# Kernel tuning notes

Hardware: AMD Instinct MI355X
Metric: run time of the kernel (lower is better)

## Reference

```python
import jax, jax.numpy as jnp
import numpy as np

B, LQ, LK = 1, 2048, 2048
D, H, KVH, DH = 4096, 32, 8, 128
G = H // KVH  # head groups


def setup_inputs() -> dict:
    key = jax.random.key(0)
    ks = jax.random.split(key, 7)
    s = 0.02
    hidden_q = jax.random.normal(ks[0], (B, LQ, D), dtype=jnp.float32)
    hidden_kv = jax.random.normal(ks[1], (B, LK, D), dtype=jnp.float32)
    # causal boolean mask (batch, len_q, len_k)
    attention_mask = jnp.broadcast_to(jnp.tril(jnp.ones((LQ, LK), dtype=bool)), (B, LQ, LK))
    position_bias = jax.random.normal(ks[2], (H, LQ, LK), dtype=jnp.float32) * 0.1
    Wq = jax.random.normal(ks[3], (D, H * DH), dtype=jnp.float32) * s
    Wk = jax.random.normal(ks[4], (D, KVH * DH), dtype=jnp.float32) * s
    Wv = jax.random.normal(ks[5], (D, KVH * DH), dtype=jnp.float32) * s
    Wo = jax.random.normal(ks[6], (H * DH, D), dtype=jnp.float32) * s
    return {"hidden_q": hidden_q, "hidden_kv": hidden_kv,
            "attention_mask": attention_mask, "position_bias": position_bias,
            "Wq": Wq, "Wk": Wk, "Wv": Wv, "Wo": Wo}


def reference(hidden_q, hidden_kv, attention_mask, position_bias, Wq, Wk, Wv, Wo):
    inv4 = DH ** -0.25  # q and k each scaled by dim_head**-1/4
    q = (hidden_q @ Wq) * inv4            # [B, LQ, H*DH]
    k = (hidden_kv @ Wk) * inv4           # [B, LK, KVH*DH]
    v = hidden_kv @ Wv                     # [B, LK, KVH*DH]
    q = q.reshape(B, LQ, KVH, G, DH)       # group heads for GQA
    k = k.reshape(B, LK, KVH, DH)
    v = v.reshape(B, LK, KVH, DH)
    # score: [B, KVH, G, LQ, LK] -> [B, H, LQ, LK]
    score = jnp.einsum('bqkgd,blkd->bkgql', q, k).reshape(B, H, LQ, LK)
    score = score + position_bias[None]
    mask = attention_mask[:, None]         # [B, 1, LQ, LK]
    score = jnp.where(mask, score, -jnp.inf)
    p = jax.nn.softmax(score, axis=-1)
    p = jnp.where(mask, p, 0.0)
    out = jnp.einsum('bkgql,blkd->bqkgd', p.reshape(B, KVH, G, LQ, LK), v)
    out = out.reshape(B, LQ, H * DH) @ Wo  # [B, LQ, D]
    return out
```

## Files before the change

kernel.cpp:

```cpp
#include <hip/hip_runtime.h>
#include <hip/hip_bf16.h>
#include <cstdint>
#include <cstddef>

typedef __attribute__((ext_vector_type(4))) float f32x4;
typedef __attribute__((ext_vector_type(4))) short s16x4;
typedef __attribute__((ext_vector_type(8))) short s16x8;

#define SLQ 2048
#define SLK 2048
#define SNH 32
#define SDH 128

__device__ __forceinline__ short f2bf(float x) {
  unsigned u = __builtin_bit_cast(unsigned, x);
  u += 0x7FFF + ((u >> 16) & 1);
  return (short)(u >> 16);
}

__device__ __forceinline__ void gload_lds16(const void* g, const void* l) {
  __builtin_amdgcn_global_load_lds((const __attribute__((address_space(1))) void*)g,
                                   (__attribute__((address_space(3))) void*)l,
                                   16, 0, 0);
}

template<int CTRL>
__device__ __forceinline__ float dpp_f32(float x) {
  return __builtin_bit_cast(float, __builtin_amdgcn_update_dpp(
      0, __builtin_bit_cast(int, x), CTRL, 0xF, 0xF, true));
}
__device__ __forceinline__ float rowmax16(float x) {
  x = fmaxf(x, dpp_f32<0x128>(x));
  x = fmaxf(x, dpp_f32<0x124>(x));
  x = fmaxf(x, dpp_f32<0x122>(x));
  x = fmaxf(x, dpp_f32<0x121>(x));
  return x;
}
__device__ __forceinline__ float rowsum16(float x) {
  x += dpp_f32<0x128>(x);
  x += dpp_f32<0x124>(x);
  x += dpp_f32<0x122>(x);
  x += dpp_f32<0x121>(x);
  return x;
}

__global__ void convert_bf16_2(const float* __restrict__ in0, short* __restrict__ out0,
                               const float* __restrict__ in1, short* __restrict__ out1) {
  const int i = blockIdx.x * 256 + threadIdx.x;
  const float* in = blockIdx.y ? in1 : in0;
  short* out = blockIdx.y ? out1 : out0;
  f32x4 a = ((const f32x4*)in)[i];
  s16x4 b;
  b[0] = f2bf(a[0]); b[1] = f2bf(a[1]); b[2] = f2bf(a[2]); b[3] = f2bf(a[3]);
  ((s16x4*)out)[i] = b;
}

__global__ void transpose_all(const float* __restrict__ Wq, const float* __restrict__ Wo,
                              const float* __restrict__ Wk, const float* __restrict__ Wv,
                              short* __restrict__ WqT, short* __restrict__ WoT,
                              short* __restrict__ WkT, short* __restrict__ WvT) {
  __shared__ short T[64][68];
  const int K = 4096;
  int bx = blockIdx.x;
  const float* W; short* Wt; int N;
  if (bx < 64)       { W = Wq; Wt = WqT; N = 4096; }
  else if (bx < 128) { W = Wo; Wt = WoT; N = 4096; bx -= 64; }
  else if (bx < 144) { W = Wk; Wt = WkT; N = 1024; bx -= 128; }
  else               { W = Wv; Wt = WvT; N = 1024; bx -= 144; }
  const int tid = threadIdx.x;
  const int k0 = blockIdx.y * 64, n0 = bx * 64;
  const int r = tid >> 4;
  const int c4 = (tid & 15) * 4;
#pragma unroll
  for (int i = 0; i < 4; ++i) {
    f32x4 a = *(const f32x4*)(W + (size_t)(k0 + r + i * 16) * N + n0 + c4);
#pragma unroll
    for (int j = 0; j < 4; ++j) T[c4 + j][r + i * 16] = f2bf(a[j]);
  }
  __syncthreads();
  const int rn = tid >> 3;
  const int c8 = (tid & 7) * 8;
#pragma unroll
  for (int i = 0; i < 2; ++i) {
    s16x4 v0 = *(const s16x4*)&T[rn + i * 32][c8];
    s16x4 v1 = *(const s16x4*)&T[rn + i * 32][c8 + 4];
    short* dst = Wt + (size_t)(n0 + rn + i * 32) * K + k0 + c8;
    *(s16x4*)dst = v0;
    *(s16x4*)(dst + 4) = v1;
  }
}

template<int CM>
__global__ __launch_bounds__(512, 1)
void gemm_big(const short* __restrict__ A, const short* __restrict__ Bt,
              void* __restrict__ Cv, float scale) {
  __shared__ short As[3][128 * 64];
  __shared__ short Bs[3][256 * 64];
  const int N = 4096, K = 4096;
  const int tid = threadIdx.x, lane = tid & 63, w = tid >> 6;
  const int l15 = lane & 15, lg = lane >> 4;
  const int wr = w >> 2, wc = w & 3;
  const int nbx = N >> 8;
  const int nwg = gridDim.x, b = blockIdx.x;
  const int wg = (b & 7) * (nwg >> 3) + (b >> 3);
  const int m0 = (wg / nbx) * 128, n0 = (wg % nbx) * 256;

  f32x4 acc[4][4];
#pragma unroll
  for (int a = 0; a < 4; ++a)
#pragma unroll
    for (int c = 0; c < 4; ++c)
      acc[a][c] = (f32x4){0.f, 0.f, 0.f, 0.f};

#define GSTAGE(T, BUF) do {                                                    \
    _Pragma("unroll") for (int i_ = 0; i_ < 2; ++i_) {                         \
      const int ci = i_ * 512 + tid, r_ = ci >> 3, c_ = ci & 7;                \
      gload_lds16(A + (size_t)(m0 + r_) * K + (T) * 64 + ((c_ ^ (r_ & 7)) * 8),\
                  (const short*)As[BUF] + ci * 8); }                           \
    _Pragma("unroll") for (int i_ = 0; i_ < 4; ++i_) {                         \
      const int ci = i_ * 512 + tid, r_ = ci >> 3, c_ = ci & 7;                \
      gload_lds16(Bt + (size_t)(n0 + r_) * K + (T) * 64 + ((c_ ^ (r_ & 7)) * 8),\
                  (const short*)Bs[BUF] + ci * 8); }                           \
  } while (0)

  const int NT = K >> 6;
  GSTAGE(0, 0); GSTAGE(1, 1); GSTAGE(2, 2);
  int buf = 0;
  for (int t = 0; t < NT; ++t) {
    if (t + 2 < NT)      asm volatile("s_waitcnt vmcnt(12)" ::: "memory");
    else if (t + 1 < NT) asm volatile("s_waitcnt vmcnt(6)" ::: "memory");
    else                 asm volatile("s_waitcnt vmcnt(0)" ::: "memory");
    __builtin_amdgcn_s_barrier();
    const short* Ab = As[buf];
    const short* Bb = Bs[buf];
    s16x8 af[2][4], bfv[2][4];
#pragma unroll
    for (int kk = 0; kk < 2; ++kk) {
#pragma unroll
      for (int mi = 0; mi < 4; ++mi) {
        const int r = wr * 64 + mi * 16 + l15;
        const int c = (kk * 4 + lg) ^ (r & 7);
        af[kk][mi] = *(const s16x8*)(Ab + (r * 8 + c) * 8);
      }
#pragma unroll
      for (int ni = 0; ni < 4; ++ni) {
        const int r = wc * 64 + ni * 16 + l15;
        const int c = (kk * 4 + lg) ^ (r & 7);
        bfv[kk][ni] = *(const s16x8*)(Bb + (r * 8 + c) * 8);
      }
    }
    __builtin_amdgcn_s_setprio(1);
#pragma unroll
    for (int kk = 0; kk < 2; ++kk)
#pragma unroll
      for (int mi = 0; mi < 4; ++mi)
#pragma unroll
        for (int ni = 0; ni < 4; ++ni)
          acc[mi][ni] = __builtin_amdgcn_mfma_f32_16x16x32_bf16(af[kk][mi], bfv[kk][ni], acc[mi][ni], 0, 0, 0);
    __builtin_amdgcn_s_setprio(0);
    __builtin_amdgcn_s_barrier();
    if (t + 3 < NT) GSTAGE(t + 3, buf);
    buf = (buf == 2) ? 0 : buf + 1;
  }
#undef GSTAGE
#pragma unroll
  for (int mi = 0; mi < 4; ++mi) {
#pragma unroll
    for (int ni = 0; ni < 4; ++ni) {
#pragma unroll
      for (int j = 0; j < 4; ++j) {
        const int rg = m0 + wr * 64 + mi * 16 + lg * 4 + j;
        const int cg = n0 + wc * 64 + ni * 16 + l15;
        const float vv = acc[mi][ni][j] * scale;
        if (CM == 0) ((short*)Cv)[(size_t)rg * N + cg] = f2bf(vv);
        else         ((float*)Cv)[(size_t)rg * N + cg] = vv;
      }
    }
  }
}

__global__ __launch_bounds__(256, 2)
void gemm_kv(const short* __restrict__ A, const short* __restrict__ Bt,
             short* __restrict__ kout, short* __restrict__ vTout, float inv4) {
  __shared__ short As[128][32];
  __shared__ short Bs[128][32];
  const int N = 2048, K = 4096;
  const int tid = threadIdx.x, lane = tid & 63, wid = tid >> 6;
  const int l15 = lane & 15, lg = lane >> 4;
  const int nbx = N >> 7;
  const int nwg = gridDim.x, b = blockIdx.x;
  const int wg = (b & 7) * (nwg >> 3) + (b >> 3);
  const int m0 = (wg / nbx) * 128, n0 = (wg % nbx) * 128;
  const int wm = (wid >> 1) * 64, wn = (wid & 1) * 64;

  f32x4 acc[4][4];
#pragma unroll
  for (int a = 0; a < 4; ++a)
#pragma unroll
    for (int c = 0; c < 4; ++c)
      acc[a][c] = (f32x4){0.f, 0.f, 0.f, 0.f};

  for (int k0 = 0; k0 < K; k0 += 32) {
#pragma unroll
    for (int i = 0; i < 2; ++i) {
      const int c = i * 256 + wid * 64 + lane;
      const int rr = c >> 2, hh = (c & 3) * 8;
      gload_lds16(A  + (size_t)(m0 + rr) * K + k0 + hh,
                  (const short*)As + (size_t)(i * 256 + wid * 64) * 8);
      gload_lds16(Bt + (size_t)(n0 + rr) * K + k0 + hh,
                  (const short*)Bs + (size_t)(i * 256 + wid * 64) * 8);
    }
    __syncthreads();
    s16x8 af[4], bf[4];
#pragma unroll
    for (int mi = 0; mi < 4; ++mi)
      af[mi] = *(const s16x8*)&As[wm + mi * 16 + l15][lg * 8];
#pragma unroll
    for (int ni = 0; ni < 4; ++ni)
      bf[ni] = *(const s16x8*)&Bs[wn + ni * 16 + l15][lg * 8];
#pragma unroll
    for (int mi = 0; mi < 4; ++mi)
#pragma unroll
      for (int ni = 0; ni < 4; ++ni)
        acc[mi][ni] = __builtin_amdgcn_mfma_f32_16x16x32_bf16(af[mi], bf[ni], acc[mi][ni], 0, 0, 0);
    __syncthreads();
  }
  if (n0 < 1024) {
#pragma unroll
    for (int mi = 0; mi < 4; ++mi)
#pragma unroll
      for (int ni = 0; ni < 4; ++ni)
#pragma unroll
        for (int j = 0; j < 4; ++j) {
          const int rg = m0 + wm + mi * 16 + lg * 4 + j;
          const int cg = n0 + wn + ni * 16 + l15;
          kout[(size_t)rg * 1024 + cg] = f2bf(acc[mi][ni][j] * inv4);
        }
  } else {
#pragma unroll
    for (int mi = 0; mi < 4; ++mi)
#pragma unroll
      for (int ni = 0; ni < 4; ++ni) {
        s16x4 wv;
#pragma unroll
        for (int j = 0; j < 4; ++j) wv[j] = f2bf(acc[mi][ni][j]);
        const int rg0 = m0 + wm + mi * 16 + lg * 4;
        const int cg = n0 + wn + ni * 16 + l15 - 1024;
        *(s16x4*)(vTout + (size_t)cg * 2048 + rg0) = wv;
      }
  }
}

__global__ __launch_bounds__(256, 2)
void attn_kernel(const short* __restrict__ q, const short* __restrict__ k,
                 const short* __restrict__ vT, const float* __restrict__ bias,
                 short* __restrict__ o) {
  __shared__ __align__(16) short Ks[64 * 128];
  __shared__ __align__(16) short Vs[2][128 * 64];
  __shared__ __align__(16) short Ps[4][16][72];
  const int tid = threadIdx.x, lane = tid & 63, w = tid >> 6;
  const int l15 = lane & 15, lg = lane >> 4;
  const int b = blockIdx.x;
  const int h = b & 31;
  const int qt = 31 - (b >> 5);
  const int kvh = h >> 2;
  const int nt = qt + 1;

#define STAGE_K(IT) do { const int kv0_ = (IT) * 64;                          \
    _Pragma("unroll") for (int i_ = 0; i_ < 4; ++i_) {                        \
      const int ci = i_ * 256 + tid, r_ = ci >> 4, c_ = ci & 15;              \
      gload_lds16(k + (size_t)(kv0_ + r_) * 1024 + kvh * 128 + ((c_ ^ (r_ & 7)) * 8), \
                  (const short*)Ks + ci * 8); } } while (0)

#define STAGE_V(IT, P) do { const int kv0_ = (IT) * 64;                       \
    _Pragma("unroll") for (int i_ = 0; i_ < 4; ++i_) {                        \
      const int ci = i_ * 256 + tid, r_ = ci >> 3, c_ = ci & 7;               \
      gload_lds16(vT + (size_t)(kvh * 128 + r_) * 2048 + kv0_ + ((c_ ^ (r_ & 7)) * 8), \
                  (const short*)Vs[P] + ci * 8); } } while (0)

  const int qrow0 = qt * 64 + w * 16 + lg * 4;

#define LOAD_BIAS(IT, BB) do { const float* bp_ = bias + ((size_t)h * SLQ + qrow0) * SLK + (IT) * 64 + l15; \
    _Pragma("unroll") for (int ni_ = 0; ni_ < 4; ++ni_)                       \
      _Pragma("unroll") for (int j_ = 0; j_ < 4; ++j_)                        \
        BB[ni_][j_] = bp_[(size_t)j_ * SLK + ni_ * 16]; } while (0)

  s16x8 qf[4];
  {
    const short* qp = q + (size_t)(qt * 64 + w * 16 + l15) * (SNH * SDH) + h * SDH + lg * 8;
#pragma unroll
    for (int kk = 0; kk < 4; ++kk) qf[kk] = *(const s16x8*)(qp + kk * 32);
  }
  float mrow[4], lrow[4];
  f32x4 oacc[8];
#pragma unroll
  for (int j = 0; j < 4; ++j) { mrow[j] = -1e30f; lrow[j] = 0.f; }
#pragma unroll
  for (int nd = 0; nd < 8; ++nd) oacc[nd] = (f32x4){0.f, 0.f, 0.f, 0.f};

  float bbA[4][4], bbB[4][4];

  STAGE_V(0, 0);
  STAGE_K(0);
  LOAD_BIAS(0, bbA);
  if (nt > 1) LOAD_BIAS(1, bbB);

#define BODY(IT, BB) do {                                                     \
    const int p_ = (IT) & 1;                                                  \
    const int kv0_ = (IT) * 64;                                               \
    if ((IT) + 1 < nt) asm volatile("s_waitcnt vmcnt(16)" ::: "memory");      \
    else               asm volatile("s_waitcnt vmcnt(0)"  ::: "memory");      \
    __builtin_amdgcn_s_barrier();                                             \
    if ((IT) + 1 < nt) STAGE_V((IT) + 1, p_ ^ 1);                             \
    f32x4 s[4];                                                               \
    __builtin_amdgcn_s_setprio(1);                                            \
    _Pragma("unroll") for (int ni = 0; ni < 4; ++ni) {                        \
      s[ni] = (f32x4){0.f, 0.f, 0.f, 0.f};                                    \
      const int r = ni * 16 + l15;                                            \
      _Pragma("unroll") for (int kk = 0; kk < 4; ++kk) {                      \
        const int cc = kk * 4 + lg;                                           \
        s16x8 kf = *(const s16x8*)(Ks + (r * 16 + (cc ^ (r & 7))) * 8);       \
        s[ni] = __builtin_amdgcn_mfma_f32_16x16x32_bf16(qf[kk], kf, s[ni], 0, 0, 0); \
      }                                                                       \
    }                                                                         \
    __builtin_amdgcn_s_setprio(0);                                            \
    _Pragma("unroll") for (int ni = 0; ni < 4; ++ni) {                        \
      _Pragma("unroll") for (int j = 0; j < 4; ++j) {                         \
        float sv = s[ni][j] + BB[ni][j];                                      \
        if ((IT) == qt && kv0_ + ni * 16 + l15 > qrow0 + j) sv = -1e30f;      \
        s[ni][j] = sv;                                                        \
      }                                                                       \
    }                                                                         \
    float pmax[4];                                                            \
    _Pragma("unroll") for (int j = 0; j < 4; ++j) {                           \
      float mx = fmaxf(fmaxf(s[0][j], s[1][j]), fmaxf(s[2][j], s[3][j]));     \
      pmax[j] = rowmax16(mx);                                                 \
    }                                                                         \
    bool need = (pmax[0] > mrow[0] + 8.f) | (pmax[1] > mrow[1] + 8.f) |       \
                (pmax[2] > mrow[2] + 8.f) | (pmax[3] > mrow[3] + 8.f);        \
    if (__any(need)) {                                                        \
      _Pragma("unroll") for (int j = 0; j < 4; ++j) {                         \
        const float mn = fmaxf(mrow[j], pmax[j]);                             \
        const float fsj = __expf(mrow[j] - mn);                               \
        mrow[j] = mn;                                                         \
        lrow[j] *= fsj;                                                       \
        _Pragma("unroll") for (int nd = 0; nd < 8; ++nd) oacc[nd][j] *= fsj;  \
      }                                                                       \
    }                                                                         \
    float ps[4] = {0.f, 0.f, 0.f, 0.f};                                       \
    _Pragma("unroll") for (int ni = 0; ni < 4; ++ni)                          \
      _Pragma("unroll") for (int j = 0; j < 4; ++j) {                         \
        const float pv = __expf(s[ni][j] - mrow[j]);                          \
        s[ni][j] = pv;                                                        \
        ps[j] += pv;                                                          \
      }                                                                       \
    _Pragma("unroll") for (int j = 0; j < 4; ++j) lrow[j] += rowsum16(ps[j]); \
    __builtin_amdgcn_s_barrier();                                             \
    if ((IT) + 1 < nt) STAGE_K((IT) + 1);                                     \
    if ((IT) + 2 < nt) LOAD_BIAS((IT) + 2, BB);                               \
    _Pragma("unroll") for (int ni = 0; ni < 4; ++ni)                          \
      _Pragma("unroll") for (int j = 0; j < 4; ++j)                           \
        Ps[w][lg * 4 + j][ni * 16 + l15] = f2bf(s[ni][j]);                    \
    __builtin_amdgcn_s_setprio(1);                                            \
    _Pragma("unroll") for (int kk2 = 0; kk2 < 2; ++kk2) {                     \
      s16x8 pa = *(const s16x8*)&Ps[w][l15][kk2 * 32 + lg * 8];               \
      _Pragma("unroll") for (int nd = 0; nd < 8; ++nd) {                      \
        const int r = nd * 16 + l15;                                          \
        const int cc = kk2 * 4 + lg;                                          \
        s16x8 vf = *(const s16x8*)(Vs[p_] + (r * 8 + (cc ^ (r & 7))) * 8);    \
        oacc[nd] = __builtin_amdgcn_mfma_f32_16x16x32_bf16(pa, vf, oacc[nd], 0, 0, 0); \
      }                                                                       \
    }                                                                         \
    __builtin_amdgcn_s_setprio(0);                                            \
  } while (0)

  for (int it = 0; it < nt; ) {
    BODY(it, bbA);
    ++it;
    if (it < nt) { BODY(it, bbB); ++it; }
  }
#undef BODY
#undef STAGE_K
#undef STAGE_V
#undef LOAD_BIAS

#pragma unroll
  for (int j = 0; j < 4; ++j) {
    const float inv = 1.f / lrow[j];
    short* op = o + (size_t)(qrow0 + j) * (SNH * SDH) + h * SDH + l15;
#pragma unroll
    for (int nd = 0; nd < 8; ++nd)
      op[nd * 16] = f2bf(oacc[nd][j] * inv);
  }
}

extern "C" void kernel_launch(void* const* d_in, const int* in_sizes, int n_in,
                              void* d_out, int out_size, void* d_ws, size_t ws_size,
                              hipStream_t stream) {
  (void)in_sizes; (void)n_in; (void)out_size; (void)ws_size;
  const float* hq   = (const float*)d_in[0];
  const float* hkv  = (const float*)d_in[1];
  const float* bias = (const float*)d_in[3];
  const float* Wq   = (const float*)d_in[4];
  const float* Wk   = (const float*)d_in[5];
  const float* Wv   = (const float*)d_in[6];
  const float* Wo   = (const float*)d_in[7];

  short* ws = (short*)d_ws;
  const size_t MEG = 1048576;
  short* hqb  = ws;
  short* hkvb = ws + 8 * MEG;
  short* WT   = ws + 16 * MEG;
  short* WoT  = ws + 32 * MEG;
  short* WkvT = ws + 48 * MEG;
  short* qb   = ws + 56 * MEG;
  short* kb   = ws + 64 * MEG;
  short* vbT  = ws + 66 * MEG;
  short* ob   = hqb;

  const float inv4 = 0.29730177875068026f;

  convert_bf16_2<<<dim3(8192, 2), 256, 0, stream>>>(hq, hqb, hkv, hkvb);
  transpose_all<<<dim3(160, 64), 256, 0, stream>>>(
      Wq, Wo, Wk, Wv, WT, WoT, WkvT, WkvT + (size_t)1024 * 4096);

  gemm_big<0><<<256, 512, 0, stream>>>(hqb, WT, qb, inv4);
  gemm_kv<<<256, 256, 0, stream>>>(hkvb, WkvT, kb, vbT, inv4);

  attn_kernel<<<1024, 256, 0, stream>>>(qb, kb, vbT, bias, ob);

  gemm_big<1><<<256, 512, 0, stream>>>(ob, WoT, (float*)d_out, 1.0f);
}
```

Before: 472.7 us.

## Process two query heads per attention block sharing K/V tiles

The attention kernel now has each block handle two heads of the same KV group. K and V tiles loaded into LDS are reused across both heads, and the grid is halved to 512 blocks. The weight transpose and input conversion kernels are split into separate launches so the Wo workspace can be reused, and the GEMM tile-to-block mapping is changed to a fixed XCD-aware layout. This trades extra register pressure and fewer blocks for less K/V traffic, plus a few more kernel launches.

```diff
diff --git a/kernel.cpp b/kernel.cpp
--- a/kernel.cpp
+++ b/kernel.cpp
@@ -44,31 +44,21 @@
   return x;
 }
 
-__global__ void convert_bf16_2(const float* __restrict__ in0, short* __restrict__ out0,
-                               const float* __restrict__ in1, short* __restrict__ out1) {
-  const int i = blockIdx.x * 256 + threadIdx.x;
-  const float* in = blockIdx.y ? in1 : in0;
-  short* out = blockIdx.y ? out1 : out0;
-  f32x4 a = ((const f32x4*)in)[i];
-  s16x4 b;
-  b[0] = f2bf(a[0]); b[1] = f2bf(a[1]); b[2] = f2bf(a[2]); b[3] = f2bf(a[3]);
-  ((s16x4*)out)[i] = b;
-}
-
-__global__ void transpose_all(const float* __restrict__ Wq, const float* __restrict__ Wo,
-                              const float* __restrict__ Wk, const float* __restrict__ Wv,
-                              short* __restrict__ WqT, short* __restrict__ WoT,
-                              short* __restrict__ WkT, short* __restrict__ WvT) {
+__global__ void convert_bf16(const float* __restrict__ in, short* __restrict__ out, int n4) {
+  int i = blockIdx.x * 256 + threadIdx.x;
+  if (i < n4) {
+    f32x4 a = ((const f32x4*)in)[i];
+    s16x4 b;
+    b[0] = f2bf(a[0]); b[1] = f2bf(a[1]); b[2] = f2bf(a[2]); b[3] = f2bf(a[3]);
+    ((s16x4*)out)[i] = b;
+  }
+}
+
+__global__ void transpose_convert(const float* __restrict__ W, short* __restrict__ Wt,
+                                  int K, int N) {
   __shared__ short T[64][68];
-  const int K = 4096;
-  int bx = blockIdx.x;
-  const float* W; short* Wt; int N;
-  if (bx < 64)       { W = Wq; Wt = WqT; N = 4096; }
-  else if (bx < 128) { W = Wo; Wt = WoT; N = 4096; bx -= 64; }
-  else if (bx < 144) { W = Wk; Wt = WkT; N = 1024; bx -= 128; }
-  else               { W = Wv; Wt = WvT; N = 1024; bx -= 144; }
   const int tid = threadIdx.x;
-  const int k0 = blockIdx.y * 64, n0 = bx * 64;
+  const int k0 = blockIdx.y * 64, n0 = blockIdx.x * 64;
   const int r = tid >> 4;
   const int c4 = (tid & 15) * 4;
 #pragma unroll
@@ -100,10 +90,10 @@
   const int tid = threadIdx.x, lane = tid & 63, w = tid >> 6;
   const int l15 = lane & 15, lg = lane >> 4;
   const int wr = w >> 2, wc = w & 3;
-  const int nbx = N >> 8;
-  const int nwg = gridDim.x, b = blockIdx.x;
-  const int wg = (b & 7) * (nwg >> 3) + (b >> 3);
-  const int m0 = (wg / nbx) * 128, n0 = (wg % nbx) * 256;
+  const int b = blockIdx.x;
+  const int cp = b & 7, wi = b >> 3;
+  const int m0 = (wi >> 1) * 128;
+  const int n0 = (cp * 2 + (wi & 1)) * 256;
 
   f32x4 acc[4][4];
 #pragma unroll
@@ -261,9 +251,11 @@
   const int tid = threadIdx.x, lane = tid & 63, w = tid >> 6;
   const int l15 = lane & 15, lg = lane >> 4;
   const int b = blockIdx.x;
-  const int h = b & 31;
-  const int qt = 31 - (b >> 5);
-  const int kvh = h >> 2;
+  const int hp = b & 15;
+  const int qt = 31 - (b >> 4);
+  const int kvh = hp >> 1;
+  const int hA = kvh * 4 + (hp & 1) * 2;
+  const int hB = hA + 1;
   const int nt = qt + 1;
 
 #define STAGE_K(IT) do { const int kv0_ = (IT) * 64;                          \
@@ -280,39 +272,40 @@
 
   const int qrow0 = qt * 64 + w * 16 + lg * 4;
 
-#define LOAD_BIAS(IT, BB) do { const float* bp_ = bias + ((size_t)h * SLQ + qrow0) * SLK + (IT) * 64 + l15; \
+  float bbA[4][4], bbB[4][4];
+#define LOAD_BIAS(IT, BB, H) do { const float* bp_ = bias + ((size_t)(H) * SLQ + qrow0) * SLK + (IT) * 64 + l15; \
     _Pragma("unroll") for (int ni_ = 0; ni_ < 4; ++ni_)                       \
       _Pragma("unroll") for (int j_ = 0; j_ < 4; ++j_)                        \
         BB[ni_][j_] = bp_[(size_t)j_ * SLK + ni_ * 16]; } while (0)
 
-  s16x8 qf[4];
+  s16x8 qfA[4], qfB[4];
   {
-    const short* qp = q + (size_t)(qt * 64 + w * 16 + l15) * (SNH * SDH) + h * SDH + lg * 8;
-#pragma unroll
-    for (int kk = 0; kk < 4; ++kk) qf[kk] = *(const s16x8*)(qp + kk * 32);
-  }
-  float mrow[4], lrow[4];
-  f32x4 oacc[8];
-#pragma unroll
-  for (int j = 0; j < 4; ++j) { mrow[j] = -1e30f; lrow[j] = 0.f; }
-#pragma unroll
-  for (int nd = 0; nd < 8; ++nd) oacc[nd] = (f32x4){0.f, 0.f, 0.f, 0.f};
-
-  float bbA[4][4], bbB[4][4];
+    const short* qp = q + (size_t)(qt * 64 + w * 16 + l15) * (SNH * SDH) + lg * 8;
+#pragma unroll
+    for (int kk = 0; kk < 4; ++kk) {
+      qfA[kk] = *(const s16x8*)(qp + hA * SDH + kk * 32);
+      qfB[kk] = *(const s16x8*)(qp + hB * SDH + kk * 32);
+    }
+  }
+  float mrowA[4], lrowA[4], mrowB[4], lrowB[4];
+  f32x4 oaccA[8], oaccB[8];
+#pragma unroll
+  for (int j = 0; j < 4; ++j) {
+    mrowA[j] = -1e30f; lrowA[j] = 0.f;
+    mrowB[j] = -1e30f; lrowB[j] = 0.f;
+  }
+#pragma unroll
+  for (int nd = 0; nd < 8; ++nd) {
+    oaccA[nd] = (f32x4){0.f, 0.f, 0.f, 0.f};
+    oaccB[nd] = (f32x4){0.f, 0.f, 0.f, 0.f};
+  }
 
   STAGE_V(0, 0);
   STAGE_K(0);
-  LOAD_BIAS(0, bbA);
-  if (nt > 1) LOAD_BIAS(1, bbB);
-
-#define BODY(IT, BB) do {                                                     \
-    const int p_ = (IT) & 1;                                                  \
-    const int kv0_ = (IT) * 64;                                               \
-    if ((IT) + 1 < nt) asm volatile("s_waitcnt vmcnt(16)" ::: "memory");      \
-    else               asm volatile("s_waitcnt vmcnt(0)"  ::: "memory");      \
-    __builtin_amdgcn_s_barrier();                                             \
-    if ((IT) + 1 < nt) STAGE_V((IT) + 1, p_ ^ 1);                             \
-    f32x4 s[4];                                                               \
+  LOAD_BIAS(0, bbA, hA);
+  LOAD_BIAS(0, bbB, hB);
+
+#define QK_SM(QF, BB, MROW, LROW, OACC) do {                                  \
     __builtin_amdgcn_s_setprio(1);                                            \
     _Pragma("unroll") for (int ni = 0; ni < 4; ++ni) {                        \
       s[ni] = (f32x4){0.f, 0.f, 0.f, 0.f};                                    \
@@ -320,14 +313,14 @@
       _Pragma("unroll") for (int kk = 0; kk < 4; ++kk) {                      \
         const int cc = kk * 4 + lg;                                           \
         s16x8 kf = *(const s16x8*)(Ks + (r * 16 + (cc ^ (r & 7))) * 8);       \
-        s[ni] = __builtin_amdgcn_mfma_f32_16x16x32_bf16(qf[kk], kf, s[ni], 0, 0, 0); \
+        s[ni] = __builtin_amdgcn_mfma_f32_16x16x32_bf16(QF[kk], kf, s[ni], 0, 0, 0); \
       }                                                                       \
     }                                                                         \
     __builtin_amdgcn_s_setprio(0);                                            \
     _Pragma("unroll") for (int ni = 0; ni < 4; ++ni) {                        \
       _Pragma("unroll") for (int j = 0; j < 4; ++j) {                         \
         float sv = s[ni][j] + BB[ni][j];                                      \
-        if ((IT) == qt && kv0_ + ni * 16 + l15 > qrow0 + j) sv = -1e30f;      \
+        if (it == qt && kv0 + ni * 16 + l15 > qrow0 + j) sv = -1e30f;         \
         s[ni][j] = sv;                                                        \
       }                                                                       \
     }                                                                         \
@@ -336,61 +329,81 @@
       float mx = fmaxf(fmaxf(s[0][j], s[1][j]), fmaxf(s[2][j], s[3][j]));     \
       pmax[j] = rowmax16(mx);                                                 \
     }                                                                         \
-    bool need = (pmax[0] > mrow[0] + 8.f) | (pmax[1] > mrow[1] + 8.f) |       \
-                (pmax[2] > mrow[2] + 8.f) | (pmax[3] > mrow[3] + 8.f);        \
+    bool need = (pmax[0] > MROW[0] + 8.f) | (pmax[1] > MROW[1] + 8.f) |       \
+                (pmax[2] > MROW[2] + 8.f) | (pmax[3] > MROW[3] + 8.f);        \
     if (__any(need)) {                                                        \
       _Pragma("unroll") for (int j = 0; j < 4; ++j) {                         \
-        const float mn = fmaxf(mrow[j], pmax[j]);                             \
-        const float fsj = __expf(mrow[j] - mn);                               \
-        mrow[j] = mn;                                                         \
-        lrow[j] *= fsj;                                                       \
-        _Pragma("unroll") for (int nd = 0; nd < 8; ++nd) oacc[nd][j] *= fsj;  \
+        const float mn = fmaxf(MROW[j], pmax[j]);                             \
+        const float fsj = __expf(MROW[j] - mn);                               \
+        MROW[j] = mn;                                                         \
+        LROW[j] *= fsj;                                                       \
+        _Pragma("unroll") for (int nd = 0; nd < 8; ++nd) OACC[nd][j] *= fsj;  \
       }                                                                       \
     }                                                                         \
     float ps[4] = {0.f, 0.f, 0.f, 0.f};                                       \
     _Pragma("unroll") for (int ni = 0; ni < 4; ++ni)                          \
       _Pragma("unroll") for (int j = 0; j < 4; ++j) {                         \
-        const float pv = __expf(s[ni][j] - mrow[j]);                          \
+        const float pv = __expf(s[ni][j] - MROW[j]);                          \
         s[ni][j] = pv;                                                        \
         ps[j] += pv;                                                          \
       }                                                                       \
-    _Pragma("unroll") for (int j = 0; j < 4; ++j) lrow[j] += rowsum16(ps[j]); \
-    __builtin_amdgcn_s_barrier();                                             \
-    if ((IT) + 1 < nt) STAGE_K((IT) + 1);                                     \
-    if ((IT) + 2 < nt) LOAD_BIAS((IT) + 2, BB);                               \
+    _Pragma("unroll") for (int j = 0; j < 4; ++j) LROW[j] += rowsum16(ps[j]); \
+  } while (0)
+
+#define PV(S, OACC, P) do {                                                   \
     _Pragma("unroll") for (int ni = 0; ni < 4; ++ni)                          \
       _Pragma("unroll") for (int j = 0; j < 4; ++j)                           \
-        Ps[w][lg * 4 + j][ni * 16 + l15] = f2bf(s[ni][j]);                    \
+        Ps[w][lg * 4 + j][ni * 16 + l15] = f2bf(S[ni][j]);                    \
     __builtin_amdgcn_s_setprio(1);                                            \
     _Pragma("unroll") for (int kk2 = 0; kk2 < 2; ++kk2) {                     \
       s16x8 pa = *(const s16x8*)&Ps[w][l15][kk2 * 32 + lg * 8];               \
       _Pragma("unroll") for (int nd = 0; nd < 8; ++nd) {                      \
         const int r = nd * 16 + l15;                                          \
         const int cc = kk2 * 4 + lg;                                          \
-        s16x8 vf = *(const s16x8*)(Vs[p_] + (r * 8 + (cc ^ (r & 7))) * 8);    \
-        oacc[nd] = __builtin_amdgcn_mfma_f32_16x16x32_bf16(pa, vf, oacc[nd], 0, 0, 0); \
+        s16x8 vf = *(const s16x8*)(Vs[P] + (r * 8 + (cc ^ (r & 7))) * 8);     \
+        OACC[nd] = __builtin_amdgcn_mfma_f32_16x16x32_bf16(pa, vf, OACC[nd], 0, 0, 0); \
       }                                                                       \
     }                                                                         \
     __builtin_amdgcn_s_setprio(0);                                            \
   } while (0)
 
-  for (int it = 0; it < nt; ) {
-    BODY(it, bbA);
-    ++it;
-    if (it < nt) { BODY(it, bbB); ++it; }
-  }
-#undef BODY
+  for (int it = 0; it < nt; ++it) {
+    const int p = it & 1;
+    const int kv0 = it * 64;
+    asm volatile("s_waitcnt vmcnt(32)" ::: "memory");
+    __builtin_amdgcn_s_barrier();
+    if (it + 1 < nt) STAGE_V(it + 1, p ^ 1);
+    f32x4 s[4];
+    f32x4 sB[4];
+    QK_SM(qfA, bbA, mrowA, lrowA, oaccA);
+#pragma unroll
+    for (int ni = 0; ni < 4; ++ni) { sB[ni] = s[ni]; }
+    QK_SM(qfB, bbB, mrowB, lrowB, oaccB);
+    __builtin_amdgcn_s_barrier();
+    if (it + 1 < nt) {
+      STAGE_K(it + 1);
+      LOAD_BIAS(it + 1, bbA, hA);
+      LOAD_BIAS(it + 1, bbB, hB);
+    }
+    PV(sB, oaccA, p);
+    PV(s, oaccB, p);
+  }
+#undef QK_SM
+#undef PV
 #undef STAGE_K
 #undef STAGE_V
 #undef LOAD_BIAS
-
 #pragma unroll
   for (int j = 0; j < 4; ++j) {
-    const float inv = 1.f / lrow[j];
-    short* op = o + (size_t)(qrow0 + j) * (SNH * SDH) + h * SDH + l15;
-#pragma unroll
-    for (int nd = 0; nd < 8; ++nd)
-      op[nd * 16] = f2bf(oacc[nd][j] * inv);
+    const float invA = 1.f / lrowA[j];
+    const float invB = 1.f / lrowB[j];
+    short* opA = o + (size_t)(qrow0 + j) * (SNH * SDH) + hA * SDH + l15;
+    short* opB = o + (size_t)(qrow0 + j) * (SNH * SDH) + hB * SDH + l15;
+#pragma unroll
+    for (int nd = 0; nd < 8; ++nd) {
+      opA[nd * 16] = f2bf(oaccA[nd][j] * invA);
+      opB[nd * 16] = f2bf(oaccB[nd][j] * invB);
+    }
   }
 }
 
@@ -411,23 +424,26 @@
   short* hqb  = ws;
   short* hkvb = ws + 8 * MEG;
   short* WT   = ws + 16 * MEG;
-  short* WoT  = ws + 32 * MEG;
-  short* WkvT = ws + 48 * MEG;
-  short* qb   = ws + 56 * MEG;
-  short* kb   = ws + 64 * MEG;
-  short* vbT  = ws + 66 * MEG;
+  short* WkvT = ws + 32 * MEG;
+  short* qb   = ws + 40 * MEG;
+  short* kb   = ws + 48 * MEG;
+  short* vbT  = ws + 50 * MEG;
   short* ob   = hqb;
 
   const float inv4 = 0.29730177875068026f;
 
-  convert_bf16_2<<<dim3(8192, 2), 256, 0, stream>>>(hq, hqb, hkv, hkvb);
-  transpose_all<<<dim3(160, 64), 256, 0, stream>>>(
-      Wq, Wo, Wk, Wv, WT, WoT, WkvT, WkvT + (size_t)1024 * 4096);
-
+  convert_bf16<<<8192, 256, 0, stream>>>(hq,  hqb,  2097152);
+  convert_bf16<<<8192, 256, 0, stream>>>(hkv, hkvb, 2097152);
+
+  transpose_convert<<<dim3(64, 64), 256, 0, stream>>>(Wq, WT, 4096, 4096);
   gemm_big<0><<<256, 512, 0, stream>>>(hqb, WT, qb, inv4);
+
+  transpose_convert<<<dim3(16, 64), 256, 0, stream>>>(Wk, WkvT, 4096, 1024);
+  transpose_convert<<<dim3(16, 64), 256, 0, stream>>>(Wv, WkvT + (size_t)1024 * 4096, 4096, 1024);
   gemm_kv<<<256, 256, 0, stream>>>(hkvb, WkvT, kb, vbT, inv4);
 
-  attn_kernel<<<1024, 256, 0, stream>>>(qb, kb, vbT, bias, ob);
-
-  gemm_big<1><<<256, 512, 0, stream>>>(ob, WoT, (float*)d_out, 1.0f);
-}
+  attn_kernel<<<512, 256, 0, stream>>>(qb, kb, vbT, bias, ob);
+
+  transpose_convert<<<dim3(64, 64), 256, 0, stream>>>(Wo, WT, 4096, 4096);
+  gemm_big<1><<<256, 512, 0, stream>>>(ob, WT, (float*)d_out, 1.0f);
+}
```

Result: faster. 456.1 us (-3.5%).
